# Optimization experiments

Hardware: AMD Instinct MI355X
Metric: run time of the kernel (lower is better)

Reference implementation:

```python
import jax, jax.numpy as jnp
import numpy as np

B, T, IDIM, HDIM, K, LMAX, NLAYERS = 64, 1024, 120, 320, 72, 96, 3
LAMB = 0.1
NEG = -1e30


def lse3(a, b, c):
    m = jnp.maximum(jnp.maximum(a, b), c)
    return m + jnp.log(jnp.exp(a - m) + jnp.exp(b - m) + jnp.exp(c - m))


def _lstm_dir(x, Wih, Whh, bb):
    # x: [B,T,D] -> h: [B,T,H]; PyTorch gate order i,f,g,o
    gx = jnp.einsum('btd,gd->tbg', x, Wih) + bb  # [T,B,4H]
    def step(carry, g):
        h, c = carry
        g = g + h @ Whh.T
        i, f, gg, o = jnp.split(g, 4, axis=-1)
        c = jax.nn.sigmoid(f) * c + jax.nn.sigmoid(i) * jnp.tanh(gg)
        h = jax.nn.sigmoid(o) * jnp.tanh(c)
        return (h, c), h
    h0 = jnp.zeros((x.shape[0], HDIM), x.dtype)
    _, hs = jax.lax.scan(step, (h0, h0), gx)
    return hs.transpose(1, 0, 2)


def _rev(x, lengths):
    # reverse each sequence within its valid length (packed-sequence semantics)
    t = jnp.arange(x.shape[1])
    idx = jnp.where(t[None, :] < lengths[:, None], lengths[:, None] - 1 - t[None, :], t[None, :])
    return jnp.take_along_axis(x, idx[:, :, None], axis=1)


def _blstm_layer(x, Wih_f, Whh_f, b_f, Wih_b, Whh_b, b_b, lengths):
    hf = _lstm_dir(x, Wih_f, Whh_f, b_f)
    hb = _rev(_lstm_dir(_rev(x, lengths), Wih_b, Whh_b, b_b), lengths)
    return jnp.concatenate([hf, hb], axis=2)


def _ctc_forward(logp, labels, in_lens, lab_lens):
    # standard CTC alpha recursion (blank=0), log-space, vectorized over batch
    Bn, Tn, _ = logp.shape
    S = 2 * LMAX + 1
    ext = jnp.zeros((Bn, S), jnp.int32).at[:, 1::2].set(labels)  # blank-interleaved labels
    em = jnp.take_along_axis(logp, jnp.broadcast_to(ext[:, None, :], (Bn, Tn, S)), axis=2)
    em = em.transpose(1, 0, 2)  # [T,B,S]
    s_idx = jnp.arange(S)
    prev_lab = jnp.concatenate([jnp.full((Bn, 2), -1, jnp.int32), ext[:, :-2]], axis=1)
    can_skip = ((s_idx[None, :] % 2) == 1) & (ext != prev_lab)
    valid_s = s_idx[None, :] < (2 * lab_lens[:, None] + 1)
    alpha0 = jnp.full((Bn, S), NEG, logp.dtype)
    alpha0 = alpha0.at[:, 0].set(em[0][:, 0]).at[:, 1].set(em[0][:, 1])
    alpha0 = jnp.where(valid_s, alpha0, NEG)
    def step(alpha, inp):
        em_t, t = inp
        a2 = jnp.concatenate([jnp.full((Bn, 1), NEG, alpha.dtype), alpha[:, :-1]], axis=1)
        a3 = jnp.concatenate([jnp.full((Bn, 2), NEG, alpha.dtype), alpha[:, :-2]], axis=1)
        a3 = jnp.where(can_skip, a3, NEG)
        new = lse3(alpha, a2, a3) + em_t
        new = jnp.where(valid_s, new, NEG)
        new = jnp.where((t < in_lens)[:, None], new, alpha)  # freeze past utterance end
        return new, None
    alpha, _ = jax.lax.scan(step, alpha0, (em[1:], jnp.arange(1, Tn)))
    last = 2 * lab_lens
    aL = jnp.take_along_axis(alpha, last[:, None], axis=1)[:, 0]
    aLm1 = jnp.take_along_axis(alpha, (last - 1)[:, None], axis=1)[:, 0]
    return jnp.logaddexp(aL, aLm1)  # log p(labels | x)


def setup_inputs():
    key = jax.random.key(0)
    ks = jax.random.split(key, 12)
    H4 = 4 * HDIM
    s = 0.05
    return dict(
        logits=jax.random.normal(ks[0], (B, T, IDIM), jnp.float32),
        labels_padded=jax.random.randint(ks[1], (B, LMAX), 1, K).astype(jnp.int32),
        input_lengths=jax.random.randint(ks[2], (B,), T // 2, T + 1).astype(jnp.int32),
        label_lengths=jax.random.randint(ks[3], (B,), LMAX // 2, LMAX + 1).astype(jnp.int32),
        Wih0=jax.random.normal(ks[4], (2, H4, IDIM), jnp.float32) * s,
        Whh0=jax.random.normal(ks[5], (2, H4, HDIM), jnp.float32) * s,
        b0=jnp.zeros((2, H4), jnp.float32),
        Wih=jax.random.normal(ks[6], (NLAYERS - 1, 2, H4, 2 * HDIM), jnp.float32) * s,
        Whh=jax.random.normal(ks[7], (NLAYERS - 1, 2, H4, HDIM), jnp.float32) * s,
        b=jnp.zeros((NLAYERS - 1, 2, H4), jnp.float32),
        W_lin=jax.random.normal(ks[8], (K, 2 * HDIM), jnp.float32) * s,
        b_lin=jnp.zeros((K,), jnp.float32),
    )


def reference(logits, labels_padded, input_lengths, label_lengths, Wih0, Whh0, b0, Wih, Whh, b, W_lin, b_lin):
    # sort by input length descending (mirrors torch.sort + index_select)
    order = jnp.argsort(-input_lengths)
    logits = logits[order]
    labels_padded = labels_padded[order]
    input_lengths = input_lengths[order]
    label_lengths = label_lengths[order]
    # 3-layer BLSTM encoder
    x = _blstm_layer(logits, Wih0[0], Whh0[0], b0[0], Wih0[1], Whh0[1], b0[1], input_lengths)
    for l in range(NLAYERS - 1):
        x = _blstm_layer(x, Wih[l, 0], Whh[l, 0], b[l, 0], Wih[l, 1], Whh[l, 1], b[l, 1], input_lengths)
    netout = jax.nn.log_softmax(x @ W_lin.T + b_lin, axis=2)  # [B,T,K]
    # CTC-CRF: numerator = CTC alpha log-prob; denominator = free-running partition
    num = _ctc_forward(netout, labels_padded, input_lengths, label_lengths)
    tmask = jnp.arange(netout.shape[1])[None, :] < input_lengths[:, None]
    den = jnp.sum(jnp.where(tmask, jax.nn.logsumexp(netout, axis=2), 0.0), axis=1)
    return jnp.mean(den - (1.0 + LAMB) * num)
```

## Files before the change

kernel.cpp:

```cpp
#include <hip/hip_runtime.h>
#include <cstdint>
#include <cstddef>


typedef _Float16 f16;
typedef _Float16 h2v   __attribute__((ext_vector_type(2)));
typedef _Float16 f16x8 __attribute__((ext_vector_type(8)));
typedef float    f32x4 __attribute__((ext_vector_type(4)));

#define NEGF (-1e30f)
#define CT 128

__device__ __forceinline__ float dot2f(h2v a, h2v b, float c) {
#if __has_builtin(__builtin_amdgcn_fdot2)
  return __builtin_amdgcn_fdot2(a, b, c, false);
#else
  return c + (float)a.x * (float)b.x + (float)a.y * (float)b.y;
#endif
}

__device__ __forceinline__ void stage16(f16* lds, const f16* g) {
#if __has_builtin(__builtin_amdgcn_global_load_lds)
  __builtin_amdgcn_global_load_lds(
      (const __attribute__((address_space(1))) uint32_t*)g,
      (__attribute__((address_space(3))) uint32_t*)lds, 16, 0, 0);
#else
  int lane = threadIdx.x & 63;
  *(f16x8*)&lds[lane * 8] = *(const f16x8*)g;
#endif
}


__global__ void conv_logits(const float* __restrict__ src, f16* __restrict__ dst) {
  int idx = blockIdx.x * 256 + threadIdx.x;
  int row = idx >> 7, k = idx & 127;
  dst[idx] = (f16)((k < 120) ? src[(size_t)row * 120 + k] : 0.f);
}

__global__ void conv_wt0(const float* __restrict__ w, f16* __restrict__ dst) {
  int idx = blockIdx.x * 256 + threadIdx.x;
  int n = idx >> 7, k = idx & 127;
  dst[idx] = (f16)((k < 120) ? w[(size_t)n * 120 + k] : 0.f);
}

__global__ void conv_copy(const float* __restrict__ src, f16* __restrict__ dst, int count) {
  int idx = blockIdx.x * 256 + threadIdx.x;
  if (idx < count) dst[idx] = (f16)src[idx];
}

__global__ void conv_wtl(const float* __restrict__ w, f16* __restrict__ dst) {
  int idx = blockIdx.x * 256 + threadIdx.x;
  int n = idx / 640, k = idx % 640;
  dst[idx] = (f16)((n < 72) ? w[(size_t)n * 640 + k] : 0.f);
}

__global__ void conv_whh(const float* __restrict__ whh0, const float* __restrict__ whh,
                         uint32_t* __restrict__ dst) {
  int o = blockIdx.x * 256 + threadIdx.x;
  int tid = o & 511;
  int g  = o >> 9;
  int j  = g % 40;
  int g2 = g / 40;
  int i  = g2 % 5;
  int g3 = g2 / 5;
  int hf = g3 & 1, slot = g3 >> 1;
  int tau = i * 512 + tid;
  int lr = tau >> 2, kq = tau & 3;
  int gate = lr / 160, u = lr - gate * 160;
  int r = gate * 320 + hf * 160 + u;
  int k = kq * 80 + j * 2;
  const float* srcm = (slot < 2) ? (whh0 + ((size_t)slot * 1280 + r) * 320)
                                 : (whh  + ((size_t)(slot - 2) * 1280 + r) * 320);
  f16 lo = (f16)srcm[k], hi = (f16)srcm[k + 1];
  dst[o] = (uint32_t)__builtin_bit_cast(unsigned short, lo) |
           ((uint32_t)__builtin_bit_cast(unsigned short, hi) << 16);
}

__global__ __launch_bounds__(256)
void gemm_chunk(const f16* __restrict__ A, const f16* __restrict__ W,
                f16* __restrict__ gxc, const int* __restrict__ lens,
                int lda, int kTiles, int c0) {
  __shared__ __align__(16) f16 As[128 * 32];
  __shared__ __align__(16) f16 Ws[128 * 32];
  const int tid = threadIdx.x;
  const int lane = tid & 63, wid = tid >> 6;
  const int wm = wid >> 1, wn = wid & 1;
  const int dir = blockIdx.y >> 6, b = blockIdx.y & 63;
  const int n0 = blockIdx.x * 128;
  const int r_base = lane >> 2;
  const int c8 = (lane & 3) * 8;
  const int len = lens[b];

  f32x4 acc[4][4] = {};

  for (int kt = 0; kt < kTiles; ++kt) {
    const int k0 = kt * 32;
    __syncthreads();
#pragma unroll
    for (int hh = 0; hh < 2; ++hh) {
      const int c = wid * 2 + hh;
      const int j = c * 16 + r_base;
      const int s = c0 * CT + j;
      const int tt = dir ? ((s < len) ? (len - 1 - s) : s) : s;
      const f16* gA = A + (size_t)(b * 1024 + tt) * lda + k0 + c8;
      const f16* gW = W + (size_t)(dir * 1280 + n0 + c * 16 + r_base) * lda + k0 + c8;
      stage16(&As[c * 512], gA);
      stage16(&Ws[c * 512], gW);
    }
    __syncthreads();

    const int koff = (lane >> 4) * 8;
    f16x8 av[4], wv[4];
#pragma unroll
    for (int i = 0; i < 4; ++i)
      av[i] = *(const f16x8*)&As[(wm * 64 + i * 16 + (lane & 15)) * 32 + koff];
#pragma unroll
    for (int i = 0; i < 4; ++i)
      wv[i] = *(const f16x8*)&Ws[(wn * 64 + i * 16 + (lane & 15)) * 32 + koff];
#pragma unroll
    for (int i = 0; i < 4; ++i)
#pragma unroll
      for (int j = 0; j < 4; ++j)
        acc[i][j] = __builtin_amdgcn_mfma_f32_16x16x32_f16(av[i], wv[j], acc[i][j], 0, 0, 0);
  }

  const int r0 = (lane >> 4) * 4, cn = lane & 15;
  const size_t obase = (size_t)(dir * 64 + b) * CT;
#pragma unroll
  for (int i = 0; i < 4; ++i) {
    const int m = wm * 64 + i * 16 + r0;
#pragma unroll
    for (int j = 0; j < 4; ++j) {
      const int n = n0 + wn * 64 + j * 16 + cn;
#pragma unroll
      for (int r = 0; r < 4; ++r)
        gxc[(obase + m + r) * 1280 + n] = (f16)acc[i][j][r];
    }
  }
}

__global__ __launch_bounds__(512, 2)
void lstm_scan_chunk(const uint32_t* __restrict__ wbuf,
                     const f16* __restrict__ gxc,
                     const float* __restrict__ bias,
                     const int* __restrict__ lens,
                     f16* __restrict__ xnext,
                     uint32_t* __restrict__ xq,
                     f16* __restrict__ hsave,
                     float* __restrict__ csave,
                     int layer, int c0) {
  const int wg = blockIdx.x;
  const int half = wg >> 7;
  const int bd = wg & 127;
  const int b = bd >> 1, dir = bd & 1;
  const int tid = threadIdx.x;

  __shared__ __align__(16) f16 hbuf[320];
  __shared__ float ylds[640];

  h2v w[5][40];
  {
    const uint32_t* wb = wbuf + (size_t)((layer * 2 + dir) * 2 + half) * 200 * 512;
#pragma unroll
    for (int i = 0; i < 5; ++i)
#pragma unroll
      for (int j = 0; j < 40; ++j)
        w[i][j] = __builtin_bit_cast(h2v, wb[(i * 40 + j) * 512 + tid]);
  }
  if (tid < 320) hbuf[tid] = (c0 == 0) ? (f16)0.f : hsave[bd * 320 + tid];

  const int len = lens[b];
  const int kq = tid & 3;
  const int qi = tid >> 2;
  const int gu = half * 160 + tid;
  float c_state = 0.f;
  float bi = 0.f, bff = 0.f, bg = 0.f, bo = 0.f;
  if (tid < 160) {
    if (c0 > 0) c_state = csave[wg * 160 + tid];
    const float* bp = bias + dir * 1280 + gu;
    bi = bp[0]; bff = bp[320]; bg = bp[640]; bo = bp[960];
  }
  __syncthreads();

  const size_t grow0 = (size_t)(dir * 64 + b) * CT;

  for (int tl = 0; tl < CT; ++tl) {
    const int s = c0 * CT + tl;
    const int tt = (dir == 0) ? s : ((s < len) ? (len - 1 - s) : s);
    float gxi = 0.f, gxf = 0.f, gxg = 0.f, gxo = 0.f;
    if (tid < 160) {
      const f16* gp = gxc + (grow0 + tl) * 1280 + gu;
      gxi = (float)gp[0]; gxf = (float)gp[320]; gxg = (float)gp[640]; gxo = (float)gp[960];
    }

    float a0 = 0.f, a1 = 0.f, a2 = 0.f, a3 = 0.f, a4 = 0.f;
    const h2v* h2 = (const h2v*)hbuf;
#pragma unroll
    for (int jb = 0; jb < 5; ++jb) {
      h2v hr[8];
#pragma unroll
      for (int j = 0; j < 8; ++j) hr[j] = h2[kq * 40 + jb * 8 + j];
#pragma unroll
      for (int j = 0; j < 8; ++j) {
        a0 = dot2f(w[0][jb * 8 + j], hr[j], a0);
        a1 = dot2f(w[1][jb * 8 + j], hr[j], a1);
        a2 = dot2f(w[2][jb * 8 + j], hr[j], a2);
        a3 = dot2f(w[3][jb * 8 + j], hr[j], a3);
        a4 = dot2f(w[4][jb * 8 + j], hr[j], a4);
      }
    }
    {
      float av[5] = {a0, a1, a2, a3, a4};
#pragma unroll
      for (int i = 0; i < 5; ++i) {
        float v = av[i];
        v += __shfl_xor(v, 1, 64);
        v += __shfl_xor(v, 2, 64);
        if (kq == 0) ylds[i * 128 + qi] = v;
      }
    }
    __syncthreads();

    const unsigned target = (unsigned)(layer * 1024 + s + 1);
    if (tid < 160) {
      const int u = tid;
      float pi = ylds[u]       + gxi + bi;
      float pf = ylds[160 + u] + gxf + bff;
      float pg = ylds[320 + u] + gxg + bg;
      float po = ylds[480 + u] + gxo + bo;
      float ig = 1.f / (1.f + expf(-pi));
      float fg = 1.f / (1.f + expf(-pf));
      float gg = tanhf(pg);
      float og = 1.f / (1.f + expf(-po));
      c_state = fg * c_state + ig * gg;
      float hv = og * tanhf(c_state);
      const f16 hh = (f16)hv;
      const uint32_t word = (target << 16) |
                            (uint32_t)__builtin_bit_cast(unsigned short, hh);
      __hip_atomic_exchange(&xq[((bd * 2 + half) * 2 + (s & 1)) * 160 + u], word,
                            __ATOMIC_RELAXED, __HIP_MEMORY_SCOPE_AGENT);
      xnext[(size_t)(b * 1024 + tt) * 640 + dir * 320 + gu] = hh;
      hbuf[gu] = hh;
      uint32_t pw;
      int spins = 0;
      do {
        pw = __hip_atomic_fetch_add(&xq[((bd * 2 + (1 - half)) * 2 + (s & 1)) * 160 + u],
                                    0u, __ATOMIC_RELAXED, __HIP_MEMORY_SCOPE_AGENT);
      } while ((pw >> 16) != target && ++spins < 200000);
      hbuf[(1 - half) * 160 + u] =
          __builtin_bit_cast(f16, (unsigned short)(pw & 0xffffu));
    }
    __syncthreads();
  }

  if (tid < 160) {
    hsave[bd * 320 + gu] = hbuf[gu];
    csave[wg * 160 + tid] = c_state;
  }
}

__global__ __launch_bounds__(256)
void gemm_proj(const f16* __restrict__ A, const f16* __restrict__ W,
               float* __restrict__ outf, int lda, int kTiles, int ldo) {
  __shared__ __align__(16) f16 As[128 * 32];
  __shared__ __align__(16) f16 Ws[128 * 32];
  const int tid = threadIdx.x;
  const int lane = tid & 63, wid = tid >> 6;
  const int wm = wid >> 1, wn = wid & 1;
  const int m0 = blockIdx.y * 128, n0 = blockIdx.x * 128;
  const int r_base = lane >> 2;
  const int c8 = (lane & 3) * 8;

  f32x4 acc[4][4] = {};

  for (int kt = 0; kt < kTiles; ++kt) {
    const int k0 = kt * 32;
    __syncthreads();
#pragma unroll
    for (int hh = 0; hh < 2; ++hh) {
      const int c = wid * 2 + hh;
      const f16* gA = A + (size_t)(m0 + c * 16 + r_base) * lda + k0 + c8;
      const f16* gW = W + (size_t)(n0 + c * 16 + r_base) * lda + k0 + c8;
      stage16(&As[c * 512], gA);
      stage16(&Ws[c * 512], gW);
    }
    __syncthreads();

    const int koff = (lane >> 4) * 8;
    f16x8 av[4], wv[4];
#pragma unroll
    for (int i = 0; i < 4; ++i)
      av[i] = *(const f16x8*)&As[(wm * 64 + i * 16 + (lane & 15)) * 32 + koff];
#pragma unroll
    for (int i = 0; i < 4; ++i)
      wv[i] = *(const f16x8*)&Ws[(wn * 64 + i * 16 + (lane & 15)) * 32 + koff];
#pragma unroll
    for (int i = 0; i < 4; ++i)
#pragma unroll
      for (int j = 0; j < 4; ++j)
        acc[i][j] = __builtin_amdgcn_mfma_f32_16x16x32_f16(av[i], wv[j], acc[i][j], 0, 0, 0);
  }

  const int r0 = (lane >> 4) * 4, cn = lane & 15;
#pragma unroll
  for (int i = 0; i < 4; ++i) {
    const int m = m0 + wm * 64 + i * 16 + r0;
#pragma unroll
    for (int j = 0; j < 4; ++j) {
      const int n = n0 + wn * 64 + j * 16 + cn;
#pragma unroll
      for (int r = 0; r < 4; ++r)
        outf[(size_t)(m + r) * ldo + n] = acc[i][j][r];
    }
  }
}

__global__ void lse_kernel(const float* __restrict__ Z, const float* __restrict__ b_lin,
                           float* __restrict__ lseout) {
  int row = blockIdx.x * 4 + (threadIdx.x >> 6);
  int l = threadIdx.x & 63;
  const float* z = Z + (size_t)row * 128;
  float v0 = (l < 72) ? z[l] + b_lin[l] : NEGF;
  float v1 = (l < 8) ? z[l + 64] + b_lin[l + 64] : NEGF;
  float m = fmaxf(v0, v1);
#pragma unroll
  for (int o = 32; o; o >>= 1) m = fmaxf(m, __shfl_xor(m, o, 64));
  float s = ((l < 72) ? expf(v0 - m) : 0.f) + ((l < 8) ? expf(v1 - m) : 0.f);
#pragma unroll
  for (int o = 32; o; o >>= 1) s += __shfl_xor(s, o, 64);
  if (l == 0) lseout[row] = m + logf(s);
}

__global__ void ctc_kernel(const float* __restrict__ Z, const float* __restrict__ lse,
                           const float* __restrict__ b_lin,
                           const int* __restrict__ labels, const int* __restrict__ inlen,
                           const int* __restrict__ lablen, float* __restrict__ num) {
  const int b = blockIdx.x;
  const int s = threadIdx.x;
  __shared__ float bufA[200], bufB[200];
  __shared__ int extS[200];
  const int S = 193;
  const int L = lablen[b], len = inlen[b];

  if (s < S) extS[s] = (s & 1) ? labels[b * 96 + (s >> 1)] : 0;
  __syncthreads();
  const int valid = (s < 2 * L + 1);
  const int e = (s < S) ? extS[s] : 0;
  int skp = 0;
  if (s < S) skp = (s & 1) && (e != ((s >= 2) ? extS[s - 2] : -1));

  if (s < S) {
    float em0 = Z[(size_t)(b * 1024) * 128 + e] + b_lin[e] - lse[b * 1024];
    float a = (s <= 1) ? em0 : NEGF;
    bufA[s] = valid ? a : NEGF;
  }
  __syncthreads();

  float* src = bufA;
  float* dst = bufB;
  for (int t = 1; t < len; ++t) {
    if (s < S) {
      float x1 = src[s];
      float x2 = (s >= 1) ? src[s - 1] : NEGF;
      float x3 = (s >= 2 && skp) ? src[s - 2] : NEGF;
      float m = fmaxf(x1, fmaxf(x2, x3));
      float l3 = m + logf(expf(x1 - m) + expf(x2 - m) + expf(x3 - m));
      float em = Z[((size_t)(b * 1024 + t)) * 128 + e] + b_lin[e] - lse[b * 1024 + t];
      dst[s] = valid ? (l3 + em) : NEGF;
    }
    __syncthreads();
    float* tmp = src; src = dst; dst = tmp;
  }
  if (s == 0) {
    int last = 2 * L;
    float aL = src[last], aLm1 = src[last - 1];
    float m = fmaxf(aL, aLm1);
    num[b] = m + logf(expf(aL - m) + expf(aLm1 - m));
  }
}

__global__ void final_kernel(const float* __restrict__ num, float* __restrict__ out) {
  int l = threadIdx.x;
  float v = -1.1f * num[l];
#pragma unroll
  for (int o = 32; o; o >>= 1) v += __shfl_xor(v, o, 64);
  if (l == 0) out[0] = v * (1.f / 64.f);
}

__global__ void sentinel_kernel(float* __restrict__ out, float code) { out[0] = code; }

extern "C" void kernel_launch(void* const* d_in, const int* in_sizes, int n_in,
                              void* d_out, int out_size, void* d_ws, size_t ws_size,
                              hipStream_t stream) {
  (void)in_sizes; (void)n_in; (void)out_size;

  const float* logits   = (const float*)d_in[0];
  const int*   labels   = (const int*)d_in[1];
  const int*   in_lens  = (const int*)d_in[2];
  const int*   lab_lens = (const int*)d_in[3];
  const float* Wih0     = (const float*)d_in[4];
  const float* Whh0     = (const float*)d_in[5];
  const float* b0       = (const float*)d_in[6];
  const float* Wih      = (const float*)d_in[7];
  const float* Whh      = (const float*)d_in[8];
  const float* bb       = (const float*)d_in[9];
  const float* W_lin    = (const float*)d_in[10];
  const float* b_lin    = (const float*)d_in[11];

  const size_t NEED = (size_t)224 * 1024 * 1024;
  if (ws_size < NEED) {
    sentinel_kernel<<<1, 1, 0, stream>>>((float*)d_out, -(float)(ws_size >> 20));
    return;
  }

  char* ws = (char*)d_ws;
  size_t off = 0;
  auto alloc = [&](size_t bytes) -> char* {
    char* p = ws + off;
    off += (bytes + 255) & ~(size_t)255;
    return p;
  };
  f16*      Xa     = (f16*)alloc((size_t)65536 * 640 * 2);
  f16*      Xb     = (f16*)alloc((size_t)65536 * 640 * 2);
  f16*      gxc    = (f16*)alloc((size_t)2 * 64 * CT * 1280 * 2);
  f16*      Wt0    = (f16*)alloc((size_t)2560 * 128 * 2);
  f16*      Wt12   = (f16*)alloc((size_t)2 * 2560 * 640 * 2);
  f16*      WtL    = (f16*)alloc((size_t)128 * 640 * 2);
  uint32_t* whh16  = (uint32_t*)alloc((size_t)6 * 2 * 200 * 512 * 4);
  float*    lseb   = (float*)alloc((size_t)65536 * 4);
  float*    num    = (float*)alloc(64 * 4);
  uint32_t* xq     = (uint32_t*)alloc((size_t)512 * 160 * 4);
  f16*      hsave  = (f16*)alloc((size_t)128 * 320 * 2);
  float*    csave  = (float*)alloc((size_t)256 * 160 * 4);
  f16*      A0     = Xb;
  float*    Z      = (float*)gxc;

  hipMemsetAsync(xq, 0, (size_t)512 * 160 * 4, stream);

  conv_logits<<<32768, 256, 0, stream>>>(logits, A0);
  conv_wt0<<<1280, 256, 0, stream>>>(Wih0, Wt0);
  conv_copy<<<12800, 256, 0, stream>>>(Wih, Wt12, 3276800);
  conv_wtl<<<320, 256, 0, stream>>>(W_lin, WtL);
  conv_whh<<<4800, 256, 0, stream>>>(Whh0, Whh, whh16);

  for (int c = 0; c < 1024 / CT; ++c) {
    gemm_chunk<<<dim3(10, 128), 256, 0, stream>>>(A0, Wt0, gxc, in_lens, 128, 4, c);
    lstm_scan_chunk<<<256, 512, 0, stream>>>(whh16, gxc, b0, in_lens, Xa, xq,
                                             hsave, csave, 0, c);
  }
  for (int c = 0; c < 1024 / CT; ++c) {
    gemm_chunk<<<dim3(10, 128), 256, 0, stream>>>(Xa, Wt12, gxc, in_lens, 640, 20, c);
    lstm_scan_chunk<<<256, 512, 0, stream>>>(whh16, gxc, bb, in_lens, Xb, xq,
                                             hsave, csave, 1, c);
  }
  for (int c = 0; c < 1024 / CT; ++c) {
    gemm_chunk<<<dim3(10, 128), 256, 0, stream>>>(Xb, Wt12 + (size_t)2560 * 640, gxc,
                                                  in_lens, 640, 20, c);
    lstm_scan_chunk<<<256, 512, 0, stream>>>(whh16, gxc, bb + 2560, in_lens, Xa, xq,
                                             hsave, csave, 2, c);
  }
  gemm_proj<<<dim3(1, 512), 256, 0, stream>>>(Xa, WtL, Z, 640, 20, 128);

  lse_kernel<<<16384, 256, 0, stream>>>(Z, b_lin, lseb);
  ctc_kernel<<<64, 256, 0, stream>>>(Z, lseb, b_lin, labels, in_lens, lab_lens, num);
  final_kernel<<<1, 64, 0, stream>>>(num, (float*)d_out);
}
```

Baseline: 9.331 ms.

## Overlap partner h exchange with own-half matvec, batch xnext stores, rewrite CTC

The LSTM scan now splits the recurrent weights by k-half. One thread group computes the contribution of its own h half while the other group polls for the partner workgroup's half, so cross-workgroup communication overlaps with compute. Exchange words are packed two-per-u64 and published at the start of the step. Per-step xnext stores are staged in LDS and flushed in vectorized batches every 32 steps. The CTC kernel becomes a single wave with 4 states per lane, register shuffles and prefetched emissions, and fast exp/log intrinsics replace precise ones, which adds some numerical risk.

```diff
diff --git a/kernel.cpp b/kernel.cpp
--- a/kernel.cpp
+++ b/kernel.cpp
@@ -7,6 +7,7 @@
 typedef _Float16 h2v   __attribute__((ext_vector_type(2)));
 typedef _Float16 f16x8 __attribute__((ext_vector_type(8)));
 typedef float    f32x4 __attribute__((ext_vector_type(4)));
+typedef unsigned long long u64;
 
 #define NEGF (-1e30f)
 #define CT 128
@@ -63,12 +64,14 @@
   int g2 = g / 40;
   int i  = g2 % 5;
   int g3 = g2 / 5;
-  int hf = g3 & 1, slot = g3 >> 1;
-  int tau = i * 512 + tid;
-  int lr = tau >> 2, kq = tau & 3;
+  int half = g3 & 1, slot = g3 >> 1;
+  int group = tid >> 8, gtid = tid & 255;
+  int ksub = gtid & 1;
+  int lr = i * 128 + (gtid >> 1);
   int gate = lr / 160, u = lr - gate * 160;
-  int r = gate * 320 + hf * 160 + u;
-  int k = kq * 80 + j * 2;
+  int r = gate * 320 + half * 160 + u;
+  int khalf = group ? (1 - half) : half;
+  int k = khalf * 160 + ksub * 80 + 2 * j;
   const float* srcm = (slot < 2) ? (whh0 + ((size_t)slot * 1280 + r) * 320)
                                  : (whh  + ((size_t)(slot - 2) * 1280 + r) * 320);
   f16 lo = (f16)srcm[k], hi = (f16)srcm[k + 1];
@@ -145,7 +148,7 @@
                      const float* __restrict__ bias,
                      const int* __restrict__ lens,
                      f16* __restrict__ xnext,
-                     uint32_t* __restrict__ xq,
+                     u64* __restrict__ xq,
                      f16* __restrict__ hsave,
                      float* __restrict__ csave,
                      int layer, int c0) {
@@ -154,9 +157,12 @@
   const int bd = wg & 127;
   const int b = bd >> 1, dir = bd & 1;
   const int tid = threadIdx.x;
+  const int group = tid >> 8, gtid = tid & 255;
 
   __shared__ __align__(16) f16 hbuf[320];
-  __shared__ float ylds[640];
+  __shared__ float yldsA[640];
+  __shared__ float yldsB[640];
+  __shared__ __align__(16) f16 hstage[64 * 160];
 
   h2v w[5][40];
   {
@@ -167,12 +173,16 @@
       for (int j = 0; j < 40; ++j)
         w[i][j] = __builtin_bit_cast(h2v, wb[(i * 40 + j) * 512 + tid]);
   }
-  if (tid < 320) hbuf[tid] = (c0 == 0) ? (f16)0.f : hsave[bd * 320 + tid];
 
   const int len = lens[b];
-  const int kq = tid & 3;
-  const int qi = tid >> 2;
   const int gu = half * 160 + tid;
+  const int khalf = group ? (1 - half) : half;
+  const int kb2 = khalf * 80 + (gtid & 1) * 40;
+  const int lrb = gtid >> 1;
+
+  if (tid < 160) {
+    hbuf[gu] = (c0 == 0) ? (f16)0.f : hsave[bd * 320 + gu];
+  }
   float c_state = 0.f;
   float bi = 0.f, bff = 0.f, bg = 0.f, bo = 0.f;
   if (tid < 160) {
@@ -183,76 +193,143 @@
   __syncthreads();
 
   const size_t grow0 = (size_t)(dir * 64 + b) * CT;
+  u64* const my_xq   = xq + ((size_t)(bd * 2 + half) * 2) * 80;
+  u64* const par_xq  = xq + ((size_t)(bd * 2 + (1 - half)) * 2) * 80;
 
   for (int tl = 0; tl < CT; ++tl) {
     const int s = c0 * CT + tl;
-    const int tt = (dir == 0) ? s : ((s < len) ? (len - 1 - s) : s);
+    const uint32_t tag = (uint32_t)(layer * 1024 + s + 1);
+
+    if (tid < 80) {
+      const uint32_t lo = ((uint32_t)tag << 16) |
+          (uint32_t)__builtin_bit_cast(unsigned short, hbuf[half * 160 + tid]);
+      const uint32_t hi = ((uint32_t)tag << 16) |
+          (uint32_t)__builtin_bit_cast(unsigned short, hbuf[half * 160 + 80 + tid]);
+      const u64 word = ((u64)hi << 32) | (u64)lo;
+      __hip_atomic_exchange(&my_xq[(s & 1) * 80 + tid], word,
+                            __ATOMIC_RELAXED, __HIP_MEMORY_SCOPE_AGENT);
+    }
     float gxi = 0.f, gxf = 0.f, gxg = 0.f, gxo = 0.f;
     if (tid < 160) {
       const f16* gp = gxc + (grow0 + tl) * 1280 + gu;
       gxi = (float)gp[0]; gxf = (float)gp[320]; gxg = (float)gp[640]; gxo = (float)gp[960];
     }
 
-    float a0 = 0.f, a1 = 0.f, a2 = 0.f, a3 = 0.f, a4 = 0.f;
+    float acc0 = 0.f, acc1 = 0.f, acc2 = 0.f, acc3 = 0.f, acc4 = 0.f;
     const h2v* h2 = (const h2v*)hbuf;
-#pragma unroll
-    for (int jb = 0; jb < 5; ++jb) {
-      h2v hr[8];
-#pragma unroll
-      for (int j = 0; j < 8; ++j) hr[j] = h2[kq * 40 + jb * 8 + j];
-#pragma unroll
-      for (int j = 0; j < 8; ++j) {
-        a0 = dot2f(w[0][jb * 8 + j], hr[j], a0);
-        a1 = dot2f(w[1][jb * 8 + j], hr[j], a1);
-        a2 = dot2f(w[2][jb * 8 + j], hr[j], a2);
-        a3 = dot2f(w[3][jb * 8 + j], hr[j], a3);
-        a4 = dot2f(w[4][jb * 8 + j], hr[j], a4);
+
+    if (group == 0) {
+#pragma unroll
+      for (int jb = 0; jb < 5; ++jb) {
+        h2v hr[8];
+#pragma unroll
+        for (int j = 0; j < 8; ++j) hr[j] = h2[kb2 + jb * 8 + j];
+#pragma unroll
+        for (int j = 0; j < 8; ++j) {
+          acc0 = dot2f(w[0][jb * 8 + j], hr[j], acc0);
+          acc1 = dot2f(w[1][jb * 8 + j], hr[j], acc1);
+          acc2 = dot2f(w[2][jb * 8 + j], hr[j], acc2);
+          acc3 = dot2f(w[3][jb * 8 + j], hr[j], acc3);
+          acc4 = dot2f(w[4][jb * 8 + j], hr[j], acc4);
+        }
       }
-    }
-    {
-      float av[5] = {a0, a1, a2, a3, a4};
-#pragma unroll
-      for (int i = 0; i < 5; ++i) {
-        float v = av[i];
-        v += __shfl_xor(v, 1, 64);
-        v += __shfl_xor(v, 2, 64);
-        if (kq == 0) ylds[i * 128 + qi] = v;
+      {
+        float av[5] = {acc0, acc1, acc2, acc3, acc4};
+#pragma unroll
+        for (int i = 0; i < 5; ++i) {
+          float v = av[i] + __shfl_xor(av[i], 1, 64);
+          if (!(tid & 1)) yldsA[i * 128 + lrb] = v;
+        }
       }
-    }
-    __syncthreads();
-
-    const unsigned target = (unsigned)(layer * 1024 + s + 1);
+    } else if (gtid < 80) {
+      u64 pw;
+      int spins = 0;
+      do {
+        pw = __hip_atomic_fetch_add(&par_xq[(s & 1) * 80 + gtid], (u64)0,
+                                    __ATOMIC_RELAXED, __HIP_MEMORY_SCOPE_AGENT);
+      } while ((((uint32_t)(pw >> 48) != tag) ||
+                ((uint32_t)((pw >> 16) & 0xffffu) != tag)) && ++spins < 200000);
+      hbuf[(1 - half) * 160 + gtid] =
+          __builtin_bit_cast(f16, (unsigned short)(pw & 0xffffu));
+      hbuf[(1 - half) * 160 + 80 + gtid] =
+          __builtin_bit_cast(f16, (unsigned short)((pw >> 32) & 0xffffu));
+    }
+    __syncthreads();
+
+    if (group == 1) {
+#pragma unroll
+      for (int jb = 0; jb < 5; ++jb) {
+        h2v hr[8];
+#pragma unroll
+        for (int j = 0; j < 8; ++j) hr[j] = h2[kb2 + jb * 8 + j];
+#pragma unroll
+        for (int j = 0; j < 8; ++j) {
+          acc0 = dot2f(w[0][jb * 8 + j], hr[j], acc0);
+          acc1 = dot2f(w[1][jb * 8 + j], hr[j], acc1);
+          acc2 = dot2f(w[2][jb * 8 + j], hr[j], acc2);
+          acc3 = dot2f(w[3][jb * 8 + j], hr[j], acc3);
+          acc4 = dot2f(w[4][jb * 8 + j], hr[j], acc4);
+        }
+      }
+      {
+        float av[5] = {acc0, acc1, acc2, acc3, acc4};
+#pragma unroll
+        for (int i = 0; i < 5; ++i) {
+          float v = av[i] + __shfl_xor(av[i], 1, 64);
+          if (!(tid & 1)) yldsB[i * 128 + lrb] = v;
+        }
+      }
+    } else if ((tl & 31) == 0 && tl > 0) {
+      const int tw = tl - 32;
+#pragma unroll
+      for (int it = 0; it < 3; ++it) {
+        const int slot = it * 256 + tid;
+        if (slot < 640) {
+          const int r = (int)(((unsigned)slot * 52429u) >> 20);
+          const int j = slot - r * 20;
+          const int sp = c0 * CT + tw + r;
+          const int ttp = dir ? ((sp < len) ? (len - 1 - sp) : sp) : sp;
+          f16x8 v = *(const f16x8*)&hstage[((tw + r) & 63) * 160 + j * 8];
+          *(f16x8*)&xnext[(size_t)(b * 1024 + ttp) * 640 + dir * 320 + half * 160 + j * 8] = v;
+        }
+      }
+    }
+    __syncthreads();
+
     if (tid < 160) {
       const int u = tid;
-      float pi = ylds[u]       + gxi + bi;
-      float pf = ylds[160 + u] + gxf + bff;
-      float pg = ylds[320 + u] + gxg + bg;
-      float po = ylds[480 + u] + gxo + bo;
-      float ig = 1.f / (1.f + expf(-pi));
-      float fg = 1.f / (1.f + expf(-pf));
+      float pi = yldsA[u]       + yldsB[u]       + gxi + bi;
+      float pf = yldsA[160 + u] + yldsB[160 + u] + gxf + bff;
+      float pg = yldsA[320 + u] + yldsB[320 + u] + gxg + bg;
+      float po = yldsA[480 + u] + yldsB[480 + u] + gxo + bo;
+      float ig = 1.f / (1.f + __expf(-pi));
+      float fg = 1.f / (1.f + __expf(-pf));
       float gg = tanhf(pg);
-      float og = 1.f / (1.f + expf(-po));
+      float og = 1.f / (1.f + __expf(-po));
       c_state = fg * c_state + ig * gg;
       float hv = og * tanhf(c_state);
       const f16 hh = (f16)hv;
-      const uint32_t word = (target << 16) |
-                            (uint32_t)__builtin_bit_cast(unsigned short, hh);
-      __hip_atomic_exchange(&xq[((bd * 2 + half) * 2 + (s & 1)) * 160 + u], word,
-                            __ATOMIC_RELAXED, __HIP_MEMORY_SCOPE_AGENT);
-      xnext[(size_t)(b * 1024 + tt) * 640 + dir * 320 + gu] = hh;
       hbuf[gu] = hh;
-      uint32_t pw;
-      int spins = 0;
-      do {
-        pw = __hip_atomic_fetch_add(&xq[((bd * 2 + (1 - half)) * 2 + (s & 1)) * 160 + u],
-                                    0u, __ATOMIC_RELAXED, __HIP_MEMORY_SCOPE_AGENT);
-      } while ((pw >> 16) != target && ++spins < 200000);
-      hbuf[(1 - half) * 160 + u] =
-          __builtin_bit_cast(f16, (unsigned short)(pw & 0xffffu));
-    }
-    __syncthreads();
-  }
-
+      hstage[(tl & 63) * 160 + u] = hh;
+    }
+    __syncthreads();
+  }
+
+  {
+    const int tw = CT - 32;
+#pragma unroll
+    for (int it = 0; it < 6; ++it) {
+      const int slot = it * 512 + tid;
+      if (slot < 640) {
+        const int r = (int)(((unsigned)slot * 52429u) >> 20);
+        const int j = slot - r * 20;
+        const int sp = c0 * CT + tw + r;
+        const int ttp = dir ? ((sp < len) ? (len - 1 - sp) : sp) : sp;
+        f16x8 v = *(const f16x8*)&hstage[((tw + r) & 63) * 160 + j * 8];
+        *(f16x8*)&xnext[(size_t)(b * 1024 + ttp) * 640 + dir * 320 + half * 160 + j * 8] = v;
+      }
+    }
+  }
   if (tid < 160) {
     hsave[bd * 320 + gu] = hbuf[gu];
     csave[wg * 160 + tid] = c_state;
@@ -325,10 +402,10 @@
   float m = fmaxf(v0, v1);
 #pragma unroll
   for (int o = 32; o; o >>= 1) m = fmaxf(m, __shfl_xor(m, o, 64));
-  float s = ((l < 72) ? expf(v0 - m) : 0.f) + ((l < 8) ? expf(v1 - m) : 0.f);
+  float s = ((l < 72) ? __expf(v0 - m) : 0.f) + ((l < 8) ? __expf(v1 - m) : 0.f);
 #pragma unroll
   for (int o = 32; o; o >>= 1) s += __shfl_xor(s, o, 64);
-  if (l == 0) lseout[row] = m + logf(s);
+  if (l == 0) lseout[row] = m + __logf(s);
 }
 
 __global__ void ctc_kernel(const float* __restrict__ Z, const float* __restrict__ lse,
@@ -336,46 +413,89 @@
                            const int* __restrict__ labels, const int* __restrict__ inlen,
                            const int* __restrict__ lablen, float* __restrict__ num) {
   const int b = blockIdx.x;
-  const int s = threadIdx.x;
-  __shared__ float bufA[200], bufB[200];
-  __shared__ int extS[200];
-  const int S = 193;
+  const int lane = threadIdx.x;
+  __shared__ int ext[200];
+  __shared__ float afin[200];
+
+  for (int s = lane; s < 200; s += 64)
+    ext[s] = (s < 193 && (s & 1)) ? labels[b * 96 + (s >> 1)] : 0;
+  __syncthreads();
+
   const int L = lablen[b], len = inlen[b];
-
-  if (s < S) extS[s] = (s & 1) ? labels[b * 96 + (s >> 1)] : 0;
+  const int Send = 2 * L + 1;
+  const float* Zb = Z + (size_t)b * 1024 * 128;
+  const float* lsb = lse + (size_t)b * 1024;
+
+  float a[4];
+  int   e[4];
+  float bl[4];
+  bool  skp[4], val[4];
+#pragma unroll
+  for (int j = 0; j < 4; ++j) {
+    const int s = lane * 4 + j;
+    e[j]   = (s < 193) ? ext[s] : 0;
+    val[j] = (s < Send) && (s < 193);
+    skp[j] = (s < 193) && (s & 1) && (s >= 2) && (ext[s] != ext[s - 2]);
+    bl[j]  = b_lin[e[j]];
+  }
+  {
+    const float ls0 = lsb[0];
+#pragma unroll
+    for (int j = 0; j < 4; ++j) {
+      const int s = lane * 4 + j;
+      a[j] = (s <= 1 && val[j]) ? (Zb[e[j]] + bl[j] - ls0) : NEGF;
+    }
+  }
+
+  float emA[4], emB[4], lsA, lsB;
+#pragma unroll
+  for (int j = 0; j < 4; ++j) emA[j] = Zb[128 + e[j]];
+  lsA = lsb[1];
+#pragma unroll
+  for (int j = 0; j < 4; ++j) emB[j] = Zb[256 + e[j]];
+  lsB = lsb[2];
+
+  for (int t = 1; t < len; ++t) {
+    float em[4];
+#pragma unroll
+    for (int j = 0; j < 4; ++j) em[j] = emA[j];
+    const float lst = lsA;
+#pragma unroll
+    for (int j = 0; j < 4; ++j) emA[j] = emB[j];
+    lsA = lsB;
+    if (t + 2 < len) {
+      const float* zr = Zb + (size_t)(t + 2) * 128;
+#pragma unroll
+      for (int j = 0; j < 4; ++j) emB[j] = zr[e[j]];
+      lsB = lsb[t + 2];
+    }
+
+    float p3 = __shfl_up(a[3], 1, 64);
+    float p2 = __shfl_up(a[2], 1, 64);
+    if (lane == 0) { p3 = NEGF; p2 = NEGF; }
+    const float x2[4] = {p3, a[0], a[1], a[2]};
+    const float x3[4] = {p2, p3, a[0], a[1]};
+#pragma unroll
+    for (int j = 0; j < 4; ++j) {
+      const float xa = a[j], xb = x2[j];
+      const float xc = skp[j] ? x3[j] : NEGF;
+      const float m = fmaxf(xa, fmaxf(xb, xc));
+      const float sum = __expf(xa - m) + __expf(xb - m) + __expf(xc - m);
+      const float nv = m + __logf(sum) + em[j] + bl[j] - lst;
+      a[j] = val[j] ? nv : NEGF;
+    }
+  }
+
+#pragma unroll
+  for (int j = 0; j < 4; ++j) {
+    const int s = lane * 4 + j;
+    if (s < 193) afin[s] = a[j];
+  }
   __syncthreads();
-  const int valid = (s < 2 * L + 1);
-  const int e = (s < S) ? extS[s] : 0;
-  int skp = 0;
-  if (s < S) skp = (s & 1) && (e != ((s >= 2) ? extS[s - 2] : -1));
-
-  if (s < S) {
-    float em0 = Z[(size_t)(b * 1024) * 128 + e] + b_lin[e] - lse[b * 1024];
-    float a = (s <= 1) ? em0 : NEGF;
-    bufA[s] = valid ? a : NEGF;
-  }
-  __syncthreads();
-
-  float* src = bufA;
-  float* dst = bufB;
-  for (int t = 1; t < len; ++t) {
-    if (s < S) {
-      float x1 = src[s];
-      float x2 = (s >= 1) ? src[s - 1] : NEGF;
-      float x3 = (s >= 2 && skp) ? src[s - 2] : NEGF;
-      float m = fmaxf(x1, fmaxf(x2, x3));
-      float l3 = m + logf(expf(x1 - m) + expf(x2 - m) + expf(x3 - m));
-      float em = Z[((size_t)(b * 1024 + t)) * 128 + e] + b_lin[e] - lse[b * 1024 + t];
-      dst[s] = valid ? (l3 + em) : NEGF;
-    }
-    __syncthreads();
-    float* tmp = src; src = dst; dst = tmp;
-  }
-  if (s == 0) {
-    int last = 2 * L;
-    float aL = src[last], aLm1 = src[last - 1];
-    float m = fmaxf(aL, aLm1);
-    num[b] = m + logf(expf(aL - m) + expf(aLm1 - m));
+  if (lane == 0) {
+    const float aL = afin[2 * L], aLm1 = afin[2 * L - 1];
+    const float m = fmaxf(aL, aLm1);
+    num[b] = m + __logf(__expf(aL - m) + __expf(aLm1 - m));
   }
 }
 
@@ -426,16 +546,16 @@
   f16*      Wt0    = (f16*)alloc((size_t)2560 * 128 * 2);
   f16*      Wt12   = (f16*)alloc((size_t)2 * 2560 * 640 * 2);
   f16*      WtL    = (f16*)alloc((size_t)128 * 640 * 2);
-  uint32_t* whh16  = (uint32_t*)alloc((size_t)6 * 2 * 200 * 512 * 4);
+  uint32_t* whh16  = (uint32_t*)alloc((size_t)12 * 5 * 40 * 512 * 4);
   float*    lseb   = (float*)alloc((size_t)65536 * 4);
   float*    num    = (float*)alloc(64 * 4);
-  uint32_t* xq     = (uint32_t*)alloc((size_t)512 * 160 * 4);
+  u64*      xq     = (u64*)alloc((size_t)512 * 80 * 8);
   f16*      hsave  = (f16*)alloc((size_t)128 * 320 * 2);
   float*    csave  = (float*)alloc((size_t)256 * 160 * 4);
   f16*      A0     = Xb;
   float*    Z      = (float*)gxc;
 
-  hipMemsetAsync(xq, 0, (size_t)512 * 160 * 4, stream);
+  hipMemsetAsync(xq, 0, (size_t)512 * 80 * 8, stream);
 
   conv_logits<<<32768, 256, 0, stream>>>(logits, A0);
   conv_wt0<<<1280, 256, 0, stream>>>(Wih0, Wt0);
@@ -462,6 +582,6 @@
   gemm_proj<<<dim3(1, 512), 256, 0, stream>>>(Xa, WtL, Z, 640, 20, 128);
 
   lse_kernel<<<16384, 256, 0, stream>>>(Z, b_lin, lseb);
-  ctc_kernel<<<64, 256, 0, stream>>>(Z, lseb, b_lin, labels, in_lens, lab_lens, num);
+  ctc_kernel<<<64, 64, 0, stream>>>(Z, lseb, b_lin, labels, in_lens, lab_lens, num);
   final_kernel<<<1, 64, 0, stream>>>(num, (float*)d_out);
 }
```

Result: slower. 12.04 ms (+29.0%).
